# Kernel tuning notes

Hardware: AMD Instinct MI355X
Metric: run time of the kernel (lower is better)

Reference implementation:

```python
import jax, jax.numpy as jnp
import numpy as np

L = 2        # num_hidden_layers
B = 2        # batch
S = 1024     # seq_len
D = 2048     # hidden_size
H = 32       # num_attention_heads
HD = D // H  # head_dim = 64
I = 8192     # intermediate_size
EPS = 1e-5
INIT = 0.02


def setup_inputs() -> dict:
    key = jax.random.key(0)
    ks = jax.random.split(key, 12)
    r = lambda k, shape: jax.random.normal(k, shape, dtype=jnp.float32) * INIT
    return {
        "hidden_states": jax.random.normal(ks[0], (B, S, D), dtype=jnp.float32),
        "attention_mask": jnp.ones((B, S), dtype=jnp.int32),
        "ln1_g": jnp.ones((L, D), jnp.float32),
        "ln1_b": jnp.zeros((L, D), jnp.float32),
        "qkv_w": r(ks[1], (L, D, 3 * D)),
        "o_w": r(ks[2], (L, D, D)),
        "ln2_g": jnp.ones((L, D), jnp.float32),
        "ln2_b": jnp.zeros((L, D), jnp.float32),
        "gu_w": r(ks[3], (L, D, 2 * I)),
        "gu_b": jnp.zeros((L, 2 * I), jnp.float32),
        "down_w": r(ks[4], (L, I, D)),
        "down_b": jnp.zeros((L, D), jnp.float32),
    }


def _layer_norm(x, g, b):
    mu = jnp.mean(x, axis=-1, keepdims=True)
    var = jnp.mean(jnp.square(x - mu), axis=-1, keepdims=True)
    return (x - mu) * jax.lax.rsqrt(var + EPS) * g + b


def _forward(hidden_states, attention_mask, ln1_g, ln1_b, qkv_w, o_w,
             ln2_g, ln2_b, gu_w, gu_b, down_w, down_b):
    # mask bias: (1 - mask) * -1e4, broadcast to [B, 1, 1, S]
    mask_bias = (1.0 - attention_mask.astype(jnp.float32))[:, None, None, :] * -10000.0
    scale = 1.0 / np.sqrt(HD)

    def layer(h, p):
        l1g, l1b, qw, ow, l2g, l2b, guw, gub, dw, db = p
        # --- attention block ---
        x = _layer_norm(h, l1g, l1b)
        qkv = jnp.einsum("bsd,de->bse", x, qw)                 # [B,S,3D]
        qkv = qkv.reshape(B, S, 3, H, HD).transpose(2, 0, 3, 1, 4)  # [3,B,H,S,HD]
        q, k, v = qkv[0], qkv[1], qkv[2]
        scores = jnp.einsum("bhqd,bhkd->bhqk", q, k) * scale + mask_bias
        attn = jax.nn.softmax(scores, axis=-1)
        ctx = jnp.einsum("bhqk,bhkd->bhqd", attn, v)           # [B,H,S,HD]
        ctx = ctx.transpose(0, 2, 1, 3).reshape(B, S, D)
        h = h + jnp.einsum("bsd,de->bse", ctx, ow)
        # --- MLP block (SwiGLU) ---
        y = _layer_norm(h, l2g, l2b)
        gu = jnp.einsum("bsd,de->bse", y, guw) + gub           # [B,S,2I]
        gate, up = gu[..., :I], gu[..., I:]
        mlp = jnp.einsum("bsi,id->bsd", jax.nn.swish(gate) * up, dw) + db
        return h + mlp, None

    params = (ln1_g, ln1_b, qkv_w, o_w, ln2_g, ln2_b, gu_w, gu_b, down_w, down_b)
    out, _ = jax.lax.scan(layer, hidden_states, params)
    return out


def reference(hidden_states, attention_mask, ln1_g, ln1_b, qkv_w, o_w,
              ln2_g, ln2_b, gu_w, gu_b, down_w, down_b):
    return _forward(hidden_states, attention_mask, ln1_g, ln1_b, qkv_w, o_w,
                    ln2_g, ln2_b, gu_w, gu_b, down_w, down_b)
```

## Files before the change

### kernel.cpp

```cpp
#include <hip/hip_runtime.h>

#define LNUM 2
#define BBATCH 2
#define SSEQ 1024
#define DDIM 2048
#define HHEADS 32
#define HDIM 64
#define IDIM 8192
#define MM 2048

typedef __attribute__((ext_vector_type(4))) float f32x4;
typedef __attribute__((ext_vector_type(8))) __bf16 bf16x8;
typedef __attribute__((ext_vector_type(4))) unsigned short us4;
typedef __attribute__((ext_vector_type(8))) unsigned short us8;

__device__ __forceinline__ unsigned short f2bf(float f) {
  union { float f; unsigned u; } v; v.f = f;
  unsigned r = v.u + 0x7fffu + ((v.u >> 16) & 1u);
  return (unsigned short)(r >> 16);
}
__device__ __forceinline__ float bf2f(unsigned short b) {
  union { unsigned u; float f; } v; v.u = ((unsigned)b) << 16;
  return v.f;
}

#define GLD16(g, l) __builtin_amdgcn_global_load_lds( \
    (const __attribute__((address_space(1))) void*)(g), \
    (__attribute__((address_space(3))) void*)(l), 16, 0, 0)

template<int REDSPLIT>
__global__ __launch_bounds__(256) void ln_kernel(
    float* __restrict__ x, const float* __restrict__ part,
    const float* __restrict__ rbias,
    const float* __restrict__ g, const float* __restrict__ bta,
    unsigned short* __restrict__ out)
{
  int tid = threadIdx.x;
  int lane = tid & 63, w = tid >> 6;
  int row = blockIdx.x;
  float* xr = x + (size_t)row * DDIM;
  f32x4* xr4 = (f32x4*)xr;
  f32x4 v[2];
  float s1 = 0.f, s2 = 0.f;
#pragma unroll
  for (int i = 0; i < 2; i++) {
    int idx4 = tid + 256 * i;
    v[i] = xr4[idx4];
    if (REDSPLIT > 0) {
#pragma unroll
      for (int s = 0; s < REDSPLIT; s++) {
        f32x4 p = *(const f32x4*)(part + (size_t)s * MM * DDIM + (size_t)row * DDIM + idx4 * 4);
        v[i] += p;
      }
      if (rbias) {
        f32x4 bv = *(const f32x4*)(rbias + idx4 * 4);
        v[i] += bv;
      }
      xr4[idx4] = v[i];
    }
#pragma unroll
    for (int j = 0; j < 4; j++) { s1 += v[i][j]; s2 += v[i][j] * v[i][j]; }
  }
#pragma unroll
  for (int m = 1; m < 64; m <<= 1) {
    s1 += __shfl_xor(s1, m);
    s2 += __shfl_xor(s2, m);
  }
  __shared__ float red[8];
  if (lane == 0) { red[w * 2] = s1; red[w * 2 + 1] = s2; }
  __syncthreads();
  s1 = red[0] + red[2] + red[4] + red[6];
  s2 = red[1] + red[3] + red[5] + red[7];
  float mu = s1 / (float)DDIM;
  float var = s2 / (float)DDIM - mu * mu;
  float rstd = rsqrtf(var + 1e-5f);
#pragma unroll
  for (int i = 0; i < 2; i++) {
    int c0 = (tid + 256 * i) * 4;
    us4 o;
#pragma unroll
    for (int j = 0; j < 4; j++)
      o[j] = f2bf((v[i][j] - mu) * rstd * g[c0 + j] + bta[c0 + j]);
    *(us4*)(out + (size_t)row * DDIM + c0) = o;
  }
}

__global__ __launch_bounds__(256) void red_kernel(
    float* __restrict__ out, const float* __restrict__ part,
    const float* __restrict__ bias)
{
  size_t i = (size_t)blockIdx.x * 256 + threadIdx.x;
  f32x4 o = ((f32x4*)out)[i];
#pragma unroll
  for (int s = 0; s < 4; s++)
    o += *(const f32x4*)(part + (size_t)s * MM * DDIM + i * 4);
  int col4 = (int)((i * 4) & (DDIM - 1));
  f32x4 bv = *(const f32x4*)(bias + col4);
  o += bv;
  ((f32x4*)out)[i] = o;
}

__global__ __launch_bounds__(256) void cvt_t_kernel(
    const float* __restrict__ W, unsigned short* __restrict__ Wt, int K, int N)
{
  __shared__ float tile[32][33];
  int t = threadIdx.x;
  int k0 = blockIdx.x << 5, n0 = blockIdx.y << 5;
  int r = t >> 3, c4 = (t & 7) << 2;
  f32x4 v = *(const f32x4*)(W + (size_t)(k0 + r) * N + n0 + c4);
  tile[r][c4 + 0] = v[0]; tile[r][c4 + 1] = v[1];
  tile[r][c4 + 2] = v[2]; tile[r][c4 + 3] = v[3];
  __syncthreads();
  us4 o;
#pragma unroll
  for (int j = 0; j < 4; j++) o[j] = f2bf(tile[c4 + j][r]);
  *(us4*)(Wt + (size_t)(n0 + r) * K + k0 + c4) = o;
}

template<int OUTMODE>
__global__ __launch_bounds__(256) void gemm_kernel(
    const unsigned short* __restrict__ A, const unsigned short* __restrict__ Bt,
    unsigned short* __restrict__ outB, float* __restrict__ outF,
    const float* __restrict__ bias, int M, int N, int K)
{
  __shared__ unsigned short As[128 * 32];
  __shared__ unsigned short Bs[128 * 32];
  int tid = threadIdx.x;
  int lane = tid & 63, w = tid >> 6;
  int m0 = blockIdx.y * 128, n0 = blockIdx.x * 128;
  int wr = w >> 1, wc = w & 1;

  f32x4 z4 = {0.f, 0.f, 0.f, 0.f};
  f32x4 acc[4][4];
#pragma unroll
  for (int i = 0; i < 4; i++)
#pragma unroll
    for (int j = 0; j < 4; j++) acc[i][j] = z4;

  int bofs0 = w * 1024 + lane * 16;
  int bofs1 = (4 + w) * 1024 + lane * 16;
  int r0 = bofs0 >> 6, c0 = (bofs0 & 63) >> 1;
  int r1 = bofs1 >> 6, c1 = (bofs1 & 63) >> 1;
  const unsigned short* a0 = A + (size_t)(m0 + r0) * K + c0;
  const unsigned short* a1 = A + (size_t)(m0 + r1) * K + c1;
  const unsigned short* b0 = Bt + (size_t)(n0 + r0) * K + c0;
  const unsigned short* b1 = Bt + (size_t)(n0 + r1) * K + c1;
  unsigned short* lA0 = As + w * 512;
  unsigned short* lA1 = As + (4 + w) * 512;
  unsigned short* lB0 = Bs + w * 512;
  unsigned short* lB1 = Bs + (4 + w) * 512;

  int arow = wr * 64 + (lane & 15);
  int brow = wc * 64 + (lane & 15);
  int koff = (lane >> 4) * 8;

  for (int kt = 0; kt < K; kt += 32) {
    __syncthreads();
    GLD16(a0 + kt, lA0);
    GLD16(a1 + kt, lA1);
    GLD16(b0 + kt, lB0);
    GLD16(b1 + kt, lB1);
    __syncthreads();
    bf16x8 af[4], bfr[4];
#pragma unroll
    for (int i = 0; i < 4; i++)
      af[i] = *(const bf16x8*)(As + (arow + i * 16) * 32 + koff);
#pragma unroll
    for (int j = 0; j < 4; j++)
      bfr[j] = *(const bf16x8*)(Bs + (brow + j * 16) * 32 + koff);
#pragma unroll
    for (int i = 0; i < 4; i++)
#pragma unroll
      for (int j = 0; j < 4; j++)
        acc[i][j] = __builtin_amdgcn_mfma_f32_16x16x32_bf16(af[i], bfr[j], acc[i][j], 0, 0, 0);
  }

  int grp = lane >> 4, l = lane & 15;
#pragma unroll
  for (int mi = 0; mi < 4; mi++) {
#pragma unroll
    for (int nj = 0; nj < 4; nj++) {
      int col = n0 + wc * 64 + nj * 16 + l;
      float bv = bias ? bias[col] : 0.f;
#pragma unroll
      for (int r = 0; r < 4; r++) {
        int row = m0 + wr * 64 + mi * 16 + grp * 4 + r;
        float v = acc[mi][nj][r] + bv;
        if (OUTMODE == 2) outF[(size_t)row * N + col] += v;
        else outB[(size_t)row * N + col] = f2bf(v);
      }
    }
  }
}

#define BAR __builtin_amdgcn_s_barrier()
#define SCHED0 __builtin_amdgcn_sched_barrier(0)
#define LGKM0 { asm volatile("s_waitcnt lgkmcnt(0)" ::: "memory"); SCHED0; }
#define VMC4 { asm volatile("s_waitcnt vmcnt(4)" ::: "memory"); SCHED0; }
#define VMC0 { asm volatile("s_waitcnt vmcnt(0)" ::: "memory"); SCHED0; }

#define STG_A(p,h,t) { \
  GLD16(pA[h][0] + (size_t)(t)*64, smem + ldsA + (p)*32768 + (h)*16384); \
  GLD16(pA[h][1] + (size_t)(t)*64, smem + ldsA + (p)*32768 + (h)*16384 + 8192); }
#define STG_B(p,h,t) { \
  GLD16(pB[h][0] + (size_t)(t)*64, smem + ldsB + (p)*32768 + (h)*16384); \
  GLD16(pB[h][1] + (size_t)(t)*64, smem + ldsB + (p)*32768 + (h)*16384 + 8192); }

#define DSR_A(p, misel, ks) { \
  _Pragma("unroll") \
  for (int mi = 0; mi < 4; mi++) \
    af[mi] = *(const bf16x8*)(smem + (p)*32768 + aRd + ((misel)*64 + mi*16)*128 + ch[ks]); }
#define DSR_B(p, ks) { \
  _Pragma("unroll") \
  for (int nj = 0; nj < 4; nj++) \
    bfr[ks][nj] = *(const bf16x8*)(smem + (p)*32768 + bRd + nj*2048 + ch[ks]); }

#define MFMA16(misel, ks) { \
  _Pragma("unroll") \
  for (int mi = 0; mi < 4; mi++) \
    _Pragma("unroll") \
    for (int nj = 0; nj < 4; nj++) \
      acc[(misel)*4+mi][nj] = __builtin_amdgcn_mfma_f32_16x16x32_bf16( \
          af[mi], bfr[ks][nj], acc[(misel)*4+mi][nj], 0, 0, 0); }

#define TILE(p, t) { \
  DSR_A(p, 0, 0); DSR_B(p, 0); \
  if ((t)+1 < NT) STG_A(1-(p), 0, (t)+1); \
  SCHED0; BAR; LGKM0; \
  __builtin_amdgcn_s_setprio(1); MFMA16(0, 0); __builtin_amdgcn_s_setprio(0); \
  SCHED0; BAR; \
  DSR_A(p, 0, 1); DSR_B(p, 1); \
  if ((t)+1 < NT) STG_A(1-(p), 1, (t)+1); \
  SCHED0; BAR; LGKM0; \
  __builtin_amdgcn_s_setprio(1); MFMA16(0, 1); __builtin_amdgcn_s_setprio(0); \
  SCHED0; BAR; \
  DSR_A(p, 1, 0); \
  if ((t)+2 < NT) STG_B(p, 0, (t)+2); \
  SCHED0; BAR; LGKM0; \
  __builtin_amdgcn_s_setprio(1); MFMA16(1, 0); __builtin_amdgcn_s_setprio(0); \
  SCHED0; BAR; \
  DSR_A(p, 1, 1); \
  if ((t)+2 < NT) STG_B(p, 1, (t)+2); \
  SCHED0; BAR; LGKM0; \
  __builtin_amdgcn_s_setprio(1); MFMA16(1, 1); __builtin_amdgcn_s_setprio(0); \
  if ((t)+2 < NT) { VMC4; } else { VMC0; } \
  SCHED0; BAR; }

template<int OUTMODE>
__global__ __launch_bounds__(512, 2) void gemm256_kernel(
    const unsigned short* __restrict__ A, const unsigned short* __restrict__ Bt,
    unsigned short* __restrict__ outB, float* __restrict__ outF,
    const float* __restrict__ bias, int M, int N, int Kstride, int Kc)
{
  extern __shared__ char smem[];
  int tid = threadIdx.x;
  int lane = tid & 63, w = tid >> 6;
  int wr = w >> 2, wc = w & 3;
  int l15 = lane & 15, grp = lane >> 4;

  int nwg = gridDim.x * gridDim.y;
  int bid = blockIdx.y * gridDim.x + blockIdx.x;
  int cpx = nwg >> 3;
  int sw = (bid & 7) * cpx + (bid >> 3);
  int bx = sw % gridDim.x, by = sw / gridDim.x;
  int m0 = by * 256, n0 = bx * 256;

  int NT = Kc >> 6;
  const unsigned short* Az = A  + (size_t)blockIdx.z * Kc;
  const unsigned short* Bz = Bt + (size_t)blockIdx.z * Kc;

  int srow = lane >> 3;
  int kcol = ((lane & 7) ^ srow) * 8;
  const unsigned short* pA[2][2];
  const unsigned short* pB[2][2];
#pragma unroll
  for (int h = 0; h < 2; h++)
#pragma unroll
    for (int i = 0; i < 2; i++) {
      pA[h][i] = Az + (size_t)(m0 + h*128 + i*64 + w*8 + srow) * Kstride + kcol;
      pB[h][i] = Bz + (size_t)(n0 + h*128 + i*64 + w*8 + srow) * Kstride + kcol;
    }
  int ldsA = w*1024 + lane*16;
  int ldsB = 65536 + w*1024 + lane*16;

  int aRd = (wr*128 + l15) * 128;
  int bRd = 65536 + (wc*64 + l15) * 128;
  int ch[2];
  ch[0] = ((0*4 + grp) ^ (l15 & 7)) * 16;
  ch[1] = ((1*4 + grp) ^ (l15 & 7)) * 16;

  f32x4 z4 = {0.f, 0.f, 0.f, 0.f};
  f32x4 acc[8][4];
#pragma unroll
  for (int i = 0; i < 8; i++)
#pragma unroll
    for (int j = 0; j < 4; j++) acc[i][j] = z4;
  bf16x8 af[4];
  bf16x8 bfr[2][4];

  STG_A(0, 0, 0); STG_A(0, 1, 0); STG_B(0, 0, 0); STG_B(0, 1, 0);
  if (NT > 1) { STG_B(1, 0, 1); STG_B(1, 1, 1); VMC4; } else { VMC0; }
  BAR;

  for (int t = 0; t < NT; t += 2) {
    TILE(0, t);
    TILE(1, t + 1);
  }

#pragma unroll
  for (int mi = 0; mi < 8; mi++) {
#pragma unroll
    for (int nj = 0; nj < 4; nj++) {
      int col = n0 + wc * 64 + nj * 16 + l15;
      float bv = (OUTMODE == 0 && bias) ? bias[col] : 0.f;
#pragma unroll
      for (int r = 0; r < 4; r++) {
        int row = m0 + wr * 128 + mi * 16 + grp * 4 + r;
        float v = acc[mi][nj][r] + bv;
        if (OUTMODE == 1)
          outF[(size_t)blockIdx.z * M * N + (size_t)row * N + col] = v;
        else
          outB[(size_t)row * N + col] = f2bf(v);
      }
    }
  }
}

__global__ __launch_bounds__(256) void attn_kernel(
    const unsigned short* __restrict__ qkv, const int* __restrict__ amask,
    unsigned short* __restrict__ ctx)
{
  __shared__ unsigned short Qs[128 * 80];
  __shared__ unsigned short Ks[128 * 80];
  __shared__ unsigned short Vt[64 * 144];
  __shared__ unsigned short Ps[128 * 144];

  int tid = threadIdx.x, lane = tid & 63, w = tid >> 6;
  int grp = lane >> 4, l = lane & 15;
  int q0 = blockIdx.x * 128;
  int bh = blockIdx.y;
  int b = bh >> 5, h = bh & 31;
  const size_t rs = 3 * DDIM;
  const unsigned short* qbase = qkv + (size_t)(b * SSEQ) * rs + h * HDIM;
  const unsigned short* kbase = qbase + DDIM;
  const unsigned short* vbase = qbase + 2 * DDIM;

#pragma unroll
  for (int i = 0; i < 4; i++) {
    int c = tid + 256 * i;
    int r = c >> 3, part = c & 7;
    us8 v = *(const us8*)(qbase + (size_t)(q0 + r) * rs + part * 8);
    *(us8*)(Qs + r * 80 + part * 8) = v;
  }

  float mrun[2][4], lrun[2][4];
  f32x4 z4 = {0.f, 0.f, 0.f, 0.f};
  f32x4 oacc[2][4];
#pragma unroll
  for (int mi = 0; mi < 2; mi++)
#pragma unroll
    for (int r = 0; r < 4; r++) { mrun[mi][r] = -1e30f; lrun[mi][r] = 0.f; }
#pragma unroll
  for (int mi = 0; mi < 2; mi++)
#pragma unroll
    for (int nj = 0; nj < 4; nj++) oacc[mi][nj] = z4;

  for (int kb = 0; kb < 8; kb++) {
    __syncthreads();
#pragma unroll
    for (int i = 0; i < 4; i++) {
      int c = tid + 256 * i;
      int r = c >> 3, part = c & 7;
      us8 v = *(const us8*)(kbase + (size_t)(kb * 128 + r) * rs + part * 8);
      *(us8*)(Ks + r * 80 + part * 8) = v;
    }
#pragma unroll
    for (int i = 0; i < 2; i++) {
      int bb = tid + 256 * i;
      int hb = bb & 15, sb = bb >> 4;
      int hd0 = hb * 4, s0 = sb * 4;
      us4 rv[4];
#pragma unroll
      for (int j = 0; j < 4; j++)
        rv[j] = *(const us4*)(vbase + (size_t)(kb * 128 + s0 + j) * rs + hd0);
      int s8 = s0 >> 3, rem = s0 & 7;
#pragma unroll
      for (int j2 = 0; j2 < 4; j2++) {
        int hd = hd0 + j2;
        us4 ov;
        ov[0] = rv[0][j2]; ov[1] = rv[1][j2]; ov[2] = rv[2][j2]; ov[3] = rv[3][j2];
        *(us4*)(Vt + hd * 144 + ((s8 ^ (hd >> 2)) * 8) + rem) = ov;
      }
    }
    __syncthreads();

    f32x4 sc[2][8];
#pragma unroll
    for (int mi = 0; mi < 2; mi++)
#pragma unroll
      for (int nj = 0; nj < 8; nj++) sc[mi][nj] = z4;
#pragma unroll
    for (int ks = 0; ks < 2; ks++) {
      bf16x8 aq[2];
#pragma unroll
      for (int mi = 0; mi < 2; mi++)
        aq[mi] = *(const bf16x8*)(Qs + (w * 32 + mi * 16 + l) * 80 + ks * 32 + grp * 8);
#pragma unroll
      for (int nj = 0; nj < 8; nj++) {
        bf16x8 bk = *(const bf16x8*)(Ks + (nj * 16 + l) * 80 + ks * 32 + grp * 8);
#pragma unroll
        for (int mi = 0; mi < 2; mi++)
          sc[mi][nj] = __builtin_amdgcn_mfma_f32_16x16x32_bf16(aq[mi], bk, sc[mi][nj], 0, 0, 0);
      }
    }
    float mb[8];
#pragma unroll
    for (int nj = 0; nj < 8; nj++) {
      int col = kb * 128 + nj * 16 + l;
      mb[nj] = (1.0f - (float)amask[b * SSEQ + col]) * -10000.0f;
    }
#pragma unroll
    for (int mi = 0; mi < 2; mi++)
#pragma unroll
      for (int nj = 0; nj < 8; nj++)
#pragma unroll
        for (int r = 0; r < 4; r++)
          sc[mi][nj][r] = sc[mi][nj][r] * 0.125f + mb[nj];

    float pm[2][4];
#pragma unroll
    for (int mi = 0; mi < 2; mi++)
#pragma unroll
      for (int r = 0; r < 4; r++) {
        float m = sc[mi][0][r];
#pragma unroll
        for (int nj = 1; nj < 8; nj++) m = fmaxf(m, sc[mi][nj][r]);
#pragma unroll
        for (int s = 1; s <= 8; s <<= 1) m = fmaxf(m, __shfl_xor(m, s));
        pm[mi][r] = m;
      }
    float corr[2][4];
#pragma unroll
    for (int mi = 0; mi < 2; mi++)
#pragma unroll
      for (int r = 0; r < 4; r++) {
        float nm = fmaxf(mrun[mi][r], pm[mi][r]);
        corr[mi][r] = __expf(mrun[mi][r] - nm);
        mrun[mi][r] = nm;
      }
    float rsum[2][4];
#pragma unroll
    for (int mi = 0; mi < 2; mi++)
#pragma unroll
      for (int r = 0; r < 4; r++) rsum[mi][r] = 0.f;
#pragma unroll
    for (int mi = 0; mi < 2; mi++)
#pragma unroll
      for (int nj = 0; nj < 8; nj++)
#pragma unroll
        for (int r = 0; r < 4; r++) {
          float p = __expf(sc[mi][nj][r] - mrun[mi][r]);
          sc[mi][nj][r] = p;
          rsum[mi][r] += p;
        }
#pragma unroll
    for (int mi = 0; mi < 2; mi++)
#pragma unroll
      for (int r = 0; r < 4; r++) {
        float s = rsum[mi][r];
#pragma unroll
        for (int m = 1; m <= 8; m <<= 1) s += __shfl_xor(s, m);
        lrun[mi][r] = lrun[mi][r] * corr[mi][r] + s;
      }
#pragma unroll
    for (int mi = 0; mi < 2; mi++)
#pragma unroll
      for (int nj = 0; nj < 4; nj++)
#pragma unroll
        for (int r = 0; r < 4; r++) oacc[mi][nj][r] *= corr[mi][r];

#pragma unroll
    for (int mi = 0; mi < 2; mi++)
#pragma unroll
      for (int nj = 0; nj < 8; nj++)
#pragma unroll
        for (int r = 0; r < 4; r++)
          Ps[(w * 32 + mi * 16 + grp * 4 + r) * 144 + nj * 16 + l] = f2bf(sc[mi][nj][r]);
    __syncthreads();

#pragma unroll
    for (int ks = 0; ks < 4; ks++) {
      bf16x8 pf[2];
#pragma unroll
      for (int mi = 0; mi < 2; mi++)
        pf[mi] = *(const bf16x8*)(Ps + (w * 32 + mi * 16 + l) * 144 + ks * 32 + grp * 8);
      int s8 = ks * 4 + grp;
#pragma unroll
      for (int nj = 0; nj < 4; nj++) {
        int hd = nj * 16 + l;
        bf16x8 vf = *(const bf16x8*)(Vt + hd * 144 + ((s8 ^ (hd >> 2)) * 8));
#pragma unroll
        for (int mi = 0; mi < 2; mi++)
          oacc[mi][nj] = __builtin_amdgcn_mfma_f32_16x16x32_bf16(pf[mi], vf, oacc[mi][nj], 0, 0, 0);
      }
    }
  }

#pragma unroll
  for (int mi = 0; mi < 2; mi++)
#pragma unroll
    for (int nj = 0; nj < 4; nj++)
#pragma unroll
      for (int r = 0; r < 4; r++) {
        int qrow = q0 + w * 32 + mi * 16 + grp * 4 + r;
        int hd = nj * 16 + l;
        float v = oacc[mi][nj][r] / lrun[mi][r];
        ctx[(size_t)(b * SSEQ + qrow) * DDIM + h * HDIM + hd] = f2bf(v);
      }
}

__global__ __launch_bounds__(256) void swiglu_kernel(
    const unsigned short* __restrict__ gu, unsigned short* __restrict__ a)
{
  size_t idx = ((size_t)blockIdx.x * 256 + threadIdx.x) * 8;
  int r = (int)(idx >> 13);
  int c = (int)(idx & 8191);
  const unsigned short* gp = gu + (size_t)r * (2 * IDIM) + c;
  us8 gv = *(const us8*)gp;
  us8 uv = *(const us8*)(gp + IDIM);
  us8 ov;
#pragma unroll
  for (int j = 0; j < 8; j++) {
    float g = bf2f(gv[j]), u = bf2f(uv[j]);
    ov[j] = f2bf(g / (1.f + __expf(-g)) * u);
  }
  *(us8*)(a + idx) = ov;
}

extern "C" void kernel_launch(void* const* d_in, const int* in_sizes, int n_in,
                              void* d_out, int out_size, void* d_ws, size_t ws_size,
                              hipStream_t stream) {
  (void)in_sizes; (void)n_in; (void)out_size; (void)ws_size;
  const float* hs    = (const float*)d_in[0];
  const int*   amask = (const int*)d_in[1];
  const float* ln1_g = (const float*)d_in[2];
  const float* ln1_b = (const float*)d_in[3];
  const float* qkv_w = (const float*)d_in[4];
  const float* o_w   = (const float*)d_in[5];
  const float* ln2_g = (const float*)d_in[6];
  const float* ln2_b = (const float*)d_in[7];
  const float* gu_w  = (const float*)d_in[8];
  const float* gu_b  = (const float*)d_in[9];
  const float* down_w = (const float*)d_in[10];
  const float* down_b = (const float*)d_in[11];
  float* out = (float*)d_out;

  char* ws = (char*)d_ws;
  unsigned short* Wt   = (unsigned short*)ws;
  unsigned short* xb   = (unsigned short*)(ws + 67108864);
  unsigned short* qkvb = (unsigned short*)(ws + 75497472);
  unsigned short* ctxb = (unsigned short*)(ws + 100663296);
  unsigned short* gub  = (unsigned short*)(ws + 109051904);
  unsigned short* ab   = qkvb;
  float* P = (float*)gub;

  hipError_t e0 = hipFuncSetAttribute(
      reinterpret_cast<const void*>(&gemm256_kernel<0>),
      hipFuncAttributeMaxDynamicSharedMemorySize, 131072);
  hipError_t e1 = hipFuncSetAttribute(
      reinterpret_cast<const void*>(&gemm256_kernel<1>),
      hipFuncAttributeMaxDynamicSharedMemorySize, 131072);
  bool use256 = (e0 == hipSuccess && e1 == hipSuccess);

  hipMemcpyAsync(out, hs, (size_t)MM * DDIM * sizeof(float),
                 hipMemcpyDeviceToDevice, stream);

  for (int lidx = 0; lidx < LNUM; lidx++) {
    if (use256 && lidx > 0)
      ln_kernel<4><<<MM, 256, 0, stream>>>(out, P, down_b + (lidx - 1) * DDIM,
          ln1_g + lidx * DDIM, ln1_b + lidx * DDIM, xb);
    else
      ln_kernel<0><<<MM, 256, 0, stream>>>(out, nullptr, nullptr,
          ln1_g + lidx * DDIM, ln1_b + lidx * DDIM, xb);

    cvt_t_kernel<<<dim3(DDIM / 32, (3 * DDIM) / 32), 256, 0, stream>>>(
        qkv_w + (size_t)lidx * DDIM * 3 * DDIM, Wt, DDIM, 3 * DDIM);
    if (use256)
      gemm256_kernel<0><<<dim3((3 * DDIM) / 256, MM / 256), 512, 131072, stream>>>(
          xb, Wt, qkvb, nullptr, nullptr, MM, 3 * DDIM, DDIM, DDIM);
    else
      gemm_kernel<0><<<dim3((3 * DDIM) / 128, MM / 128), 256, 0, stream>>>(
          xb, Wt, qkvb, nullptr, nullptr, MM, 3 * DDIM, DDIM);

    attn_kernel<<<dim3(SSEQ / 128, BBATCH * HHEADS), 256, 0, stream>>>(qkvb, amask, ctxb);

    cvt_t_kernel<<<dim3(DDIM / 32, DDIM / 32), 256, 0, stream>>>(
        o_w + (size_t)lidx * DDIM * DDIM, Wt, DDIM, DDIM);
    if (use256) {
      gemm256_kernel<1><<<dim3(DDIM / 256, MM / 256, 4), 512, 131072, stream>>>(
          ctxb, Wt, nullptr, P, nullptr, MM, DDIM, DDIM, DDIM / 4);
      ln_kernel<4><<<MM, 256, 0, stream>>>(out, P, nullptr,
          ln2_g + lidx * DDIM, ln2_b + lidx * DDIM, xb);
    } else {
      gemm_kernel<2><<<dim3(DDIM / 128, MM / 128), 256, 0, stream>>>(
          ctxb, Wt, nullptr, out, nullptr, MM, DDIM, DDIM);
      ln_kernel<0><<<MM, 256, 0, stream>>>(out, nullptr, nullptr,
          ln2_g + lidx * DDIM, ln2_b + lidx * DDIM, xb);
    }

    cvt_t_kernel<<<dim3(DDIM / 32, (2 * IDIM) / 32), 256, 0, stream>>>(
        gu_w + (size_t)lidx * DDIM * 2 * IDIM, Wt, DDIM, 2 * IDIM);
    if (use256)
      gemm256_kernel<0><<<dim3((2 * IDIM) / 256, MM / 256), 512, 131072, stream>>>(
          xb, Wt, gub, nullptr, gu_b + (size_t)lidx * 2 * IDIM, MM, 2 * IDIM, DDIM, DDIM);
    else
      gemm_kernel<0><<<dim3((2 * IDIM) / 128, MM / 128), 256, 0, stream>>>(
          xb, Wt, gub, nullptr, gu_b + (size_t)lidx * 2 * IDIM, MM, 2 * IDIM, DDIM);

    swiglu_kernel<<<(MM * IDIM / 8) / 256, 256, 0, stream>>>(gub, ab);

    cvt_t_kernel<<<dim3(IDIM / 32, DDIM / 32), 256, 0, stream>>>(
        down_w + (size_t)lidx * IDIM * DDIM, Wt, IDIM, DDIM);
    if (use256) {
      gemm256_kernel<1><<<dim3(DDIM / 256, MM / 256, 4), 512, 131072, stream>>>(
          ab, Wt, nullptr, P, nullptr, MM, DDIM, IDIM, IDIM / 4);
      if (lidx == LNUM - 1)
        red_kernel<<<(MM * DDIM / 4) / 256, 256, 0, stream>>>(
            out, P, down_b + lidx * DDIM);
    } else {
      gemm_kernel<2><<<dim3(DDIM / 128, MM / 128), 256, 0, stream>>>(
          ab, Wt, nullptr, out, down_b + lidx * DDIM, MM, DDIM, IDIM);
    }
  }
}
```

Measured before the change: 1.034 ms.

## Fuse SwiGLU into gate/up GEMM epilogue and restructure attention P staging

Permutes gate/up weight columns during the bf16 transpose so each GEMM tile holds matching gate and up columns. A new epilogue mode then applies bias, swish and multiply and writes the activated product directly. This removes the separate swiglu kernel and the full intermediate round trip through memory. The attention kernel also stages P in two halves with a smaller shared buffer, drops one barrier, and adds wave priority hints around the MFMA sections, at the cost of an extra barrier per half.

After: 952.2 us. 1.09x faster.

```diff
diff --git a/kernel.cpp b/kernel.cpp
--- a/kernel.cpp
+++ b/kernel.cpp
@@ -100,6 +100,7 @@
   ((f32x4*)out)[i] = o;
 }
 
+template<int PERM>
 __global__ __launch_bounds__(256) void cvt_t_kernel(
     const float* __restrict__ W, unsigned short* __restrict__ Wt, int K, int N)
 {
@@ -107,7 +108,12 @@
   int t = threadIdx.x;
   int k0 = blockIdx.x << 5, n0 = blockIdx.y << 5;
   int r = t >> 3, c4 = (t & 7) << 2;
-  f32x4 v = *(const f32x4*)(W + (size_t)(k0 + r) * N + n0 + c4);
+  int colbase;
+  if (PERM == 1)
+    colbase = (n0 >> 1) + (c4 & 15) + ((c4 & 16) ? (N >> 1) : 0);
+  else
+    colbase = n0 + c4;
+  f32x4 v = *(const f32x4*)(W + (size_t)(k0 + r) * N + colbase);
   tile[r][c4 + 0] = v[0]; tile[r][c4 + 1] = v[1];
   tile[r][c4 + 2] = v[2]; tile[r][c4 + 3] = v[3];
   __syncthreads();
@@ -307,20 +313,42 @@
     TILE(1, t + 1);
   }
 
-#pragma unroll
-  for (int mi = 0; mi < 8; mi++) {
-#pragma unroll
-    for (int nj = 0; nj < 4; nj++) {
-      int col = n0 + wc * 64 + nj * 16 + l15;
-      float bv = (OUTMODE == 0 && bias) ? bias[col] : 0.f;
-#pragma unroll
-      for (int r = 0; r < 4; r++) {
-        int row = m0 + wr * 128 + mi * 16 + grp * 4 + r;
-        float v = acc[mi][nj][r] + bv;
-        if (OUTMODE == 1)
-          outF[(size_t)blockIdx.z * M * N + (size_t)row * N + col] = v;
-        else
-          outB[(size_t)row * N + col] = f2bf(v);
+  if (OUTMODE == 3) {
+    int cbase = n0 + wc * 64;
+    int half = N >> 1;
+#pragma unroll
+    for (int mi = 0; mi < 8; mi++) {
+#pragma unroll
+      for (int p = 0; p < 2; p++) {
+        int jcol = (cbase >> 1) + p * 16 + l15;
+        float bg = bias[jcol];
+        float bu = bias[half + jcol];
+#pragma unroll
+        for (int r = 0; r < 4; r++) {
+          int row = m0 + wr * 128 + mi * 16 + grp * 4 + r;
+          float g = acc[mi][2 * p][r] + bg;
+          float u = acc[mi][2 * p + 1][r] + bu;
+          float sv = g / (1.f + __expf(-g)) * u;
+          outB[(size_t)row * half + jcol] = f2bf(sv);
+        }
+      }
+    }
+  } else {
+#pragma unroll
+    for (int mi = 0; mi < 8; mi++) {
+#pragma unroll
+      for (int nj = 0; nj < 4; nj++) {
+        int col = n0 + wc * 64 + nj * 16 + l15;
+        float bv = (OUTMODE == 0 && bias) ? bias[col] : 0.f;
+#pragma unroll
+        for (int r = 0; r < 4; r++) {
+          int row = m0 + wr * 128 + mi * 16 + grp * 4 + r;
+          float v = acc[mi][nj][r] + bv;
+          if (OUTMODE == 1)
+            outF[(size_t)blockIdx.z * M * N + (size_t)row * N + col] = v;
+          else
+            outB[(size_t)row * N + col] = f2bf(v);
+        }
       }
     }
   }
@@ -333,7 +361,7 @@
   __shared__ unsigned short Qs[128 * 80];
   __shared__ unsigned short Ks[128 * 80];
   __shared__ unsigned short Vt[64 * 144];
-  __shared__ unsigned short Ps[128 * 144];
+  __shared__ unsigned short Ps[128 * 80];
 
   int tid = threadIdx.x, lane = tid & 63, w = tid >> 6;
   int grp = lane >> 4, l = lane & 15;
@@ -366,7 +394,6 @@
     for (int nj = 0; nj < 4; nj++) oacc[mi][nj] = z4;
 
   for (int kb = 0; kb < 8; kb++) {
-    __syncthreads();
 #pragma unroll
     for (int i = 0; i < 4; i++) {
       int c = tid + 256 * i;
@@ -399,6 +426,7 @@
     for (int mi = 0; mi < 2; mi++)
 #pragma unroll
       for (int nj = 0; nj < 8; nj++) sc[mi][nj] = z4;
+    __builtin_amdgcn_s_setprio(1);
 #pragma unroll
     for (int ks = 0; ks < 2; ks++) {
       bf16x8 aq[2];
@@ -413,6 +441,7 @@
           sc[mi][nj] = __builtin_amdgcn_mfma_f32_16x16x32_bf16(aq[mi], bk, sc[mi][nj], 0, 0, 0);
       }
     }
+    __builtin_amdgcn_s_setprio(0);
     float mb[8];
 #pragma unroll
     for (int nj = 0; nj < 8; nj++) {
@@ -480,29 +509,35 @@
         for (int r = 0; r < 4; r++) oacc[mi][nj][r] *= corr[mi][r];
 
 #pragma unroll
-    for (int mi = 0; mi < 2; mi++)
-#pragma unroll
-      for (int nj = 0; nj < 8; nj++)
-#pragma unroll
-        for (int r = 0; r < 4; r++)
-          Ps[(w * 32 + mi * 16 + grp * 4 + r) * 144 + nj * 16 + l] = f2bf(sc[mi][nj][r]);
-    __syncthreads();
-
-#pragma unroll
-    for (int ks = 0; ks < 4; ks++) {
-      bf16x8 pf[2];
+    for (int h2 = 0; h2 < 2; h2++) {
 #pragma unroll
       for (int mi = 0; mi < 2; mi++)
-        pf[mi] = *(const bf16x8*)(Ps + (w * 32 + mi * 16 + l) * 144 + ks * 32 + grp * 8);
-      int s8 = ks * 4 + grp;
-#pragma unroll
-      for (int nj = 0; nj < 4; nj++) {
-        int hd = nj * 16 + l;
-        bf16x8 vf = *(const bf16x8*)(Vt + hd * 144 + ((s8 ^ (hd >> 2)) * 8));
+#pragma unroll
+        for (int njl = 0; njl < 4; njl++)
+#pragma unroll
+          for (int r = 0; r < 4; r++)
+            Ps[(w * 32 + mi * 16 + grp * 4 + r) * 80 + njl * 16 + l] =
+                f2bf(sc[mi][h2 * 4 + njl][r]);
+      __syncthreads();
+      __builtin_amdgcn_s_setprio(1);
+#pragma unroll
+      for (int ksl = 0; ksl < 2; ksl++) {
+        bf16x8 pf[2];
 #pragma unroll
         for (int mi = 0; mi < 2; mi++)
-          oacc[mi][nj] = __builtin_amdgcn_mfma_f32_16x16x32_bf16(pf[mi], vf, oacc[mi][nj], 0, 0, 0);
-      }
+          pf[mi] = *(const bf16x8*)(Ps + (w * 32 + mi * 16 + l) * 80 + ksl * 32 + grp * 8);
+        int s8 = (h2 * 2 + ksl) * 4 + grp;
+#pragma unroll
+        for (int nj = 0; nj < 4; nj++) {
+          int hd = nj * 16 + l;
+          bf16x8 vf = *(const bf16x8*)(Vt + hd * 144 + ((s8 ^ (hd >> 2)) * 8));
+#pragma unroll
+          for (int mi = 0; mi < 2; mi++)
+            oacc[mi][nj] = __builtin_amdgcn_mfma_f32_16x16x32_bf16(pf[mi], vf, oacc[mi][nj], 0, 0, 0);
+        }
+      }
+      __builtin_amdgcn_s_setprio(0);
+      __syncthreads();
     }
   }
 
@@ -570,7 +605,10 @@
   hipError_t e1 = hipFuncSetAttribute(
       reinterpret_cast<const void*>(&gemm256_kernel<1>),
       hipFuncAttributeMaxDynamicSharedMemorySize, 131072);
-  bool use256 = (e0 == hipSuccess && e1 == hipSuccess);
+  hipError_t e3 = hipFuncSetAttribute(
+      reinterpret_cast<const void*>(&gemm256_kernel<3>),
+      hipFuncAttributeMaxDynamicSharedMemorySize, 131072);
+  bool use256 = (e0 == hipSuccess && e1 == hipSuccess && e3 == hipSuccess);
 
   hipMemcpyAsync(out, hs, (size_t)MM * DDIM * sizeof(float),
                  hipMemcpyDeviceToDevice, stream);
@@ -583,7 +621,7 @@
       ln_kernel<0><<<MM, 256, 0, stream>>>(out, nullptr, nullptr,
           ln1_g + lidx * DDIM, ln1_b + lidx * DDIM, xb);
 
-    cvt_t_kernel<<<dim3(DDIM / 32, (3 * DDIM) / 32), 256, 0, stream>>>(
+    cvt_t_kernel<0><<<dim3(DDIM / 32, (3 * DDIM) / 32), 256, 0, stream>>>(
         qkv_w + (size_t)lidx * DDIM * 3 * DDIM, Wt, DDIM, 3 * DDIM);
     if (use256)
       gemm256_kernel<0><<<dim3((3 * DDIM) / 256, MM / 256), 512, 131072, stream>>>(
@@ -594,7 +632,7 @@
 
     attn_kernel<<<dim3(SSEQ / 128, BBATCH * HHEADS), 256, 0, stream>>>(qkvb, amask, ctxb);
 
-    cvt_t_kernel<<<dim3(DDIM / 32, DDIM / 32), 256, 0, stream>>>(
+    cvt_t_kernel<0><<<dim3(DDIM / 32, DDIM / 32), 256, 0, stream>>>(
         o_w + (size_t)lidx * DDIM * DDIM, Wt, DDIM, DDIM);
     if (use256) {
       gemm256_kernel<1><<<dim3(DDIM / 256, MM / 256, 4), 512, 131072, stream>>>(
@@ -608,18 +646,20 @@
           ln2_g + lidx * DDIM, ln2_b + lidx * DDIM, xb);
     }
 
-    cvt_t_kernel<<<dim3(DDIM / 32, (2 * IDIM) / 32), 256, 0, stream>>>(
-        gu_w + (size_t)lidx * DDIM * 2 * IDIM, Wt, DDIM, 2 * IDIM);
-    if (use256)
-      gemm256_kernel<0><<<dim3((2 * IDIM) / 256, MM / 256), 512, 131072, stream>>>(
-          xb, Wt, gub, nullptr, gu_b + (size_t)lidx * 2 * IDIM, MM, 2 * IDIM, DDIM, DDIM);
-    else
+    if (use256) {
+      cvt_t_kernel<1><<<dim3(DDIM / 32, (2 * IDIM) / 32), 256, 0, stream>>>(
+          gu_w + (size_t)lidx * DDIM * 2 * IDIM, Wt, DDIM, 2 * IDIM);
+      gemm256_kernel<3><<<dim3((2 * IDIM) / 256, MM / 256), 512, 131072, stream>>>(
+          xb, Wt, ab, nullptr, gu_b + (size_t)lidx * 2 * IDIM, MM, 2 * IDIM, DDIM, DDIM);
+    } else {
+      cvt_t_kernel<0><<<dim3(DDIM / 32, (2 * IDIM) / 32), 256, 0, stream>>>(
+          gu_w + (size_t)lidx * DDIM * 2 * IDIM, Wt, DDIM, 2 * IDIM);
       gemm_kernel<0><<<dim3((2 * IDIM) / 128, MM / 128), 256, 0, stream>>>(
           xb, Wt, gub, nullptr, gu_b + (size_t)lidx * 2 * IDIM, MM, 2 * IDIM, DDIM);
-
-    swiglu_kernel<<<(MM * IDIM / 8) / 256, 256, 0, stream>>>(gub, ab);
-
-    cvt_t_kernel<<<dim3(IDIM / 32, DDIM / 32), 256, 0, stream>>>(
+      swiglu_kernel<<<(MM * IDIM / 8) / 256, 256, 0, stream>>>(gub, ab);
+    }
+
+    cvt_t_kernel<0><<<dim3(IDIM / 32, DDIM / 32), 256, 0, stream>>>(
         down_w + (size_t)lidx * IDIM * DDIM, Wt, IDIM, DDIM);
     if (use256) {
       gemm256_kernel<1><<<dim3(DDIM / 256, MM / 256, 4), 512, 131072, stream>>>(
```
